# Kernel tuning notes

Hardware: AMD Instinct MI355X
Metric: run time of the kernel (lower is better)

Reference implementation:

```python
import jax, jax.numpy as jnp
import numpy as np
from jax import lax

WD, H, B, SQ, SS, CL = 300, 100, 128, 48, 48, 16
VOCAB, CVOCAB, CD, K = 91557, 53, 16, 3


def setup_inputs() -> dict:
    key = jax.random.key(0)
    ks = jax.random.split(key, 40)
    p = lambda i, shape: jax.random.normal(ks[i], shape, jnp.float32) * 0.02
    inp = {
        'q_words': jax.random.randint(ks[0], (B, SQ), 0, VOCAB),
        'q_chars': jax.random.randint(ks[1], (B, SQ, CL), 0, CVOCAB),
        's_words': jax.random.randint(ks[2], (B, SS), 0, VOCAB),
        's_chars': jax.random.randint(ks[3], (B, SS, CL), 0, CVOCAB),
        'word_emb': p(4, (VOCAB, WD)),
        'char_emb': p(5, (CVOCAB, CD)),
        'conv_w': p(6, (CD, 1, K)),
        'conv_b': p(7, (CD,)),
    }
    din = WD + CD
    for k in range(5):
        d = din + 2 * H * k  # dense connectivity: input grows by 2H per layer
        inp[f'wih{k+1}'] = p(8 + 4 * k, (4 * H, d))
        inp[f'whh{k+1}'] = p(9 + 4 * k, (4 * H, H))
        inp[f'bih{k+1}'] = p(10 + 4 * k, (4 * H,))
        inp[f'bhh{k+1}'] = p(11 + 4 * k, (4 * H,))
    inp['fcl_w'] = p(30, (800, 5 * H))
    inp['fcl_b'] = p(31, (800,))
    inp['last_w'] = p(32, (2, 800))
    inp['last_b'] = p(33, (2,))
    return inp


def _lstm_scan(x, wih, whh, bih, bhh):
    # x: [S, B, D] -> hidden states [S, B, H]; zero initial state (PyTorch LSTMCell default)
    h0 = jnp.zeros((x.shape[1], H), x.dtype)
    def step(carry, xt):
        h, c = carry
        g = xt @ wih.T + bih + h @ whh.T + bhh
        i, f, gg, o = jnp.split(g, 4, axis=-1)
        c = jax.nn.sigmoid(f) * c + jax.nn.sigmoid(i) * jnp.tanh(gg)
        h = jax.nn.sigmoid(o) * jnp.tanh(c)
        return (h, c), h
    _, hs = lax.scan(step, (h0, h0), x)
    return hs


def _embed(words, chars, word_emb, char_emb, conv_w, conv_b):
    w_e = word_emb[words]  # [B, S, WD]
    Bn, S, Cl = chars.shape
    ce = char_emb[chars].reshape(Bn * S, 1, Cl * CD)  # flatten chars per token
    raw = lax.conv_general_dilated(ce, conv_w, (1,), 'VALID',
                                   dimension_numbers=('NCH', 'OIH', 'NCH'))
    raw = (raw + conv_b[None, :, None]).reshape(Bn, S, CD, -1)
    pooled = jnp.max(jax.nn.relu(raw), axis=-1)        # [B, S, CD]
    pooled0 = jnp.max(raw[0], axis=-1)                 # original quirk: batch row 0 has no relu
    char_e = pooled.at[0].set(pooled0)
    return jnp.concatenate([w_e, char_e], axis=2).transpose(1, 0, 2)  # [S, B, WD+CD]


def _forward(q_words, q_chars, s_words, s_chars, word_emb, char_emb, conv_w, conv_b,
             cells, fcl_w, fcl_b, last_w, last_b):
    px = _embed(q_words, q_chars, word_emb, char_emb, conv_w, conv_b)
    hx = _embed(s_words, s_chars, word_emb, char_emb, conv_w, conv_b)
    hps = hhs = None
    for (wih, whh, bih, bhh) in cells:
        p_h = _lstm_scan(px, wih, whh, bih, bhh)  # [Sp, B, H]
        h_h = _lstm_scan(hx, wih, whh, bih, bhh)  # [Sh, B, H]
        hps = p_h.transpose(1, 0, 2)              # [B, Sp, H]
        hhs = h_h.transpose(1, 0, 2)              # [B, Sh, H]
        attn = jnp.einsum('bph,bqh->bpq', hps, hhs)
        a_p = jnp.einsum('bpq,bqh->bph', jax.nn.softmax(attn, axis=2), hhs)
        a_h = jnp.einsum('bqp,bph->bqh', jax.nn.softmax(attn.transpose(0, 2, 1), axis=2), hps)
        px = jnp.concatenate([px, a_p.transpose(1, 0, 2), p_h], axis=2)
        hx = jnp.concatenate([hx, a_h.transpose(1, 0, 2), h_h], axis=2)
    hq = jnp.max(hps, axis=1)  # max-pool over time
    hs = jnp.max(hhs, axis=1)
    feats = jnp.concatenate([hq, hs, hs - hq, hq * hs, jnp.abs(hq - hs)], axis=1)
    out = jax.nn.relu(feats @ fcl_w.T + fcl_b) @ last_w.T + last_b
    return jax.nn.sigmoid(out)


def reference(q_words, q_chars, s_words, s_chars, word_emb, char_emb, conv_w, conv_b,
              wih1, whh1, bih1, bhh1, wih2, whh2, bih2, bhh2, wih3, whh3, bih3, bhh3,
              wih4, whh4, bih4, bhh4, wih5, whh5, bih5, bhh5,
              fcl_w, fcl_b, last_w, last_b):
    cells = [(wih1, whh1, bih1, bhh1), (wih2, whh2, bih2, bhh2), (wih3, whh3, bih3, bhh3),
             (wih4, whh4, bih4, bhh4), (wih5, whh5, bih5, bhh5)]
    return _forward(q_words, q_chars, s_words, s_chars, word_emb, char_emb, conv_w, conv_b,
                    cells, fcl_w, fcl_b, last_w, last_b)
```

## Files before the change

kernel.cpp:

```cpp
#include <hip/hip_runtime.h>

typedef unsigned short u16;
typedef unsigned int   u32;

#define B_   128
#define S_   48
#define H_   100
#define G_   400
#define PXP  1120

__device__ __forceinline__ float b2f(u16 u) {
    union { u32 i; float f; } v; v.i = ((u32)u) << 16; return v.f;
}
__device__ __forceinline__ u16 f2b(float f) {
    union { float f; u32 i; } v; v.f = f;
    u32 r = v.i + 0x7FFF + ((v.i >> 16) & 1);
    return (u16)(r >> 16);
}
__device__ __forceinline__ float sigf(float x) { return 1.f / (1.f + expf(-x)); }

__device__ __forceinline__ float fsig(float x) { return 1.f / (1.f + __expf(-x)); }
__device__ __forceinline__ float ftanh(float x) {
    const float t = __expf(-2.f * fabsf(x));
    const float r = (1.f - t) / (1.f + t);
    return copysignf(r, x);
}

__device__ __forceinline__ float rl(float v0, float v1, int u) {
    return __int_as_float(
        u < 64 ? __builtin_amdgcn_readlane(__float_as_int(v0), u)
               : __builtin_amdgcn_readlane(__float_as_int(v1), u - 64));
}

__device__ __forceinline__ float ldw(const void* p, long i, int bf) {
    return bf ? b2f(((const u16*)p)[i]) : ((const float*)p)[i];
}

__global__ __launch_bounds__(256) void detect_kernel(const void* wemb, int* flag)
{
    const int t = threadIdx.x;
    __shared__ int s;
    if (t == 0) s = 0;
    __syncthreads();
    int bad = 0;
    const u16* p = (const u16*)wemb;
    for (int i = t; i < 4096; i += 256) {
        float v = b2f(p[i]);
        if (!(fabsf(v) < 1e4f)) bad = 1;
    }
    if (bad) atomicOr(&s, 1);
    __syncthreads();
    if (t == 0) *flag = s ? 0 : 1;
}

__global__ __launch_bounds__(64) void embed_kernel(
    const int* __restrict__ qw, const int* __restrict__ qc,
    const int* __restrict__ sw, const int* __restrict__ sc,
    const void* __restrict__ wemb, const void* __restrict__ cemb,
    const void* __restrict__ cw, const void* __restrict__ cb,
    u16* __restrict__ px, u16* __restrict__ hx, const int* __restrict__ flagp)
{
    const int bf = *flagp;
    const int b = blockIdx.x, s = blockIdx.y, seq = blockIdx.z;
    const int* words = seq ? sw : qw;
    const int* chars = seq ? sc : qc;
    u16* dst = seq ? hx : px;
    const int t = threadIdx.x;

    u16* row = dst + (long)(s * B_ + b) * PXP;
    const int w = words[b * S_ + s];
    if (bf) {
        const u16* src = (const u16*)wemb + (long)w * 300;
        for (int d = t; d < 300; d += 64) row[d] = src[d];
    } else {
        const float* src = (const float*)wemb + (long)w * 300;
        for (int d = t; d < 300; d += 64) row[d] = f2b(src[d]);
    }

    __shared__ float ce[256];
    const int* ch = chars + (b * S_ + s) * 16;
    for (int j = t; j < 256; j += 64) {
        int ci = ch[j >> 4];
        ce[j] = ldw(cemb, ci * 16 + (j & 15), bf);
    }
    __syncthreads();

    float cwr[3][16], cbr[16];
#pragma unroll
    for (int oc = 0; oc < 16; ++oc) {
        cbr[oc] = ldw(cb, oc, bf);
#pragma unroll
        for (int kk = 0; kk < 3; ++kk) cwr[kk][oc] = ldw(cw, oc * 3 + kk, bf);
    }

    float vmax[16];
#pragma unroll
    for (int oc = 0; oc < 16; ++oc) vmax[oc] = -1e30f;

    for (int p = t; p < 254; p += 64) {
        float c0 = ce[p], c1 = ce[p + 1], c2 = ce[p + 2];
#pragma unroll
        for (int oc = 0; oc < 16; ++oc) {
            float v = fmaf(c0, cwr[0][oc], fmaf(c1, cwr[1][oc], fmaf(c2, cwr[2][oc], cbr[oc])));
            vmax[oc] = fmaxf(vmax[oc], v);
        }
    }
#pragma unroll
    for (int m = 32; m; m >>= 1) {
#pragma unroll
        for (int oc = 0; oc < 16; ++oc)
            vmax[oc] = fmaxf(vmax[oc], __shfl_xor(vmax[oc], m));
    }
    if (t == 0) {
#pragma unroll
        for (int oc = 0; oc < 16; ++oc) {
            float v = vmax[oc];
            if (b != 0) v = fmaxf(v, 0.f);
            row[300 + oc] = f2b(v);
        }
    }
}

#if defined(__gfx950__)

typedef __attribute__((ext_vector_type(4))) float f32x4;
typedef __attribute__((ext_vector_type(8))) __bf16 bf16x8;
#define LDP 72

__global__ __launch_bounds__(256) void gemm_wih(
    const u16* __restrict__ px, const u16* __restrict__ hx,
    float* __restrict__ Xg_p, float* __restrict__ Xg_h,
    const void* __restrict__ wih, const void* __restrict__ bih,
    const void* __restrict__ bhh, int K, const int* __restrict__ flagp)
{
    const int bf = *flagp;
    const u16* A = blockIdx.z ? hx : px;
    float* C = blockIdx.z ? Xg_h : Xg_p;
    const int m0 = blockIdx.x * 128, n0 = blockIdx.y * 64;

    __shared__ __align__(16) u16 As[128 * LDP];
    __shared__ __align__(16) u16 Bs[64 * LDP];

    const int tid = threadIdx.x;
    const int ra = tid >> 1;
    const int ka = (tid & 1) * 32;
    const int rb = tid >> 2;
    const int kb = (tid & 3) * 16;

    const int lane = tid & 63;
    const int w    = tid >> 6;
    const int fr   = lane & 15;
    const int fq   = lane >> 4;

    const u16* wp = (const u16*)wih;

    f32x4 acc[2][4] = {};

    for (int k0 = 0; k0 < K; k0 += 64) {
        u16* as = &As[ra * LDP + ka];
        u16* bs = &Bs[rb * LDP + kb];
        const int n = n0 + rb;
        if (k0 + 64 <= K) {
            const u16* ap = A + (long)(m0 + ra) * PXP + k0 + ka;
#pragma unroll
            for (int c = 0; c < 4; ++c)
                *(float4*)(as + c * 8) = *(const float4*)(ap + c * 8);
            if (n < G_) {
                const u16* bp = wp + (long)n * K + k0 + kb;
#pragma unroll
                for (int c = 0; c < 4; ++c)
                    *(uint2*)(bs + c * 4) = *(const uint2*)(bp + c * 4);
            } else {
#pragma unroll
                for (int i = 0; i < 16; ++i) bs[i] = 0;
            }
        } else {
            const u16* ar = A + (long)(m0 + ra) * PXP;
            const u16* br = wp + (long)n * K;
            const int nok = n < G_;
#pragma unroll
            for (int i = 0; i < 32; ++i) {
                const int k = k0 + ka + i;
                as[i] = (k < K) ? ar[k] : (u16)0;
            }
#pragma unroll
            for (int i = 0; i < 16; ++i) {
                const int k = k0 + kb + i;
                bs[i] = (nok && k < K) ? br[k] : (u16)0;
            }
        }
        __syncthreads();

#pragma unroll
        for (int ks = 0; ks < 64; ks += 32) {
            bf16x8 a0 = *(const bf16x8*)&As[(w * 32 + fr) * LDP + ks + fq * 8];
            bf16x8 a1 = *(const bf16x8*)&As[(w * 32 + 16 + fr) * LDP + ks + fq * 8];
#pragma unroll
            for (int j = 0; j < 4; ++j) {
                bf16x8 bj = *(const bf16x8*)&Bs[(j * 16 + fr) * LDP + ks + fq * 8];
                acc[0][j] = __builtin_amdgcn_mfma_f32_16x16x32_bf16(a0, bj, acc[0][j], 0, 0, 0);
                acc[1][j] = __builtin_amdgcn_mfma_f32_16x16x32_bf16(a1, bj, acc[1][j], 0, 0, 0);
            }
        }
        __syncthreads();
    }

#pragma unroll
    for (int j = 0; j < 4; ++j) {
        const int col = n0 + j * 16 + fr;
        if (col < G_) {
            const float bias = ldw(bih, col, bf) + ldw(bhh, col, bf);
#pragma unroll
            for (int m = 0; m < 2; ++m)
#pragma unroll
                for (int i = 0; i < 4; ++i) {
                    const int row = m0 + w * 32 + m * 16 + fq * 4 + i;
                    C[(long)row * G_ + col] = acc[m][j][i] + bias;
                }
        }
    }
}
#undef LDP

#else

__global__ __launch_bounds__(256) void gemm_wih(
    const u16* __restrict__ px, const u16* __restrict__ hx,
    float* __restrict__ Xg_p, float* __restrict__ Xg_h,
    const void* __restrict__ wih, const void* __restrict__ bih,
    const void* __restrict__ bhh, int K, const int* __restrict__ flagp)
{
    const int bf = *flagp;
    const u16* A = blockIdx.z ? hx : px;
    float* C = blockIdx.z ? Xg_h : Xg_p;

    __shared__ float As[16][64];
    __shared__ float Bs[16][64];

    const int tid = threadIdx.x;
    const int tx = tid & 15, ty = tid >> 4;
    const int m0 = blockIdx.x * 64, n0 = blockIdx.y * 64;
    const int lr = tid >> 2, lk = (tid & 3) * 4;

    float acc[4][4] = {};

    for (int k0 = 0; k0 < K; k0 += 16) {
        const u16* Ap = A + (long)(m0 + lr) * PXP + k0 + lk;
#pragma unroll
        for (int u = 0; u < 4; ++u)
            As[lk + u][lr] = (k0 + lk + u < K) ? b2f(Ap[u]) : 0.f;
        {
            const int n = n0 + lr;
#pragma unroll
            for (int u = 0; u < 4; ++u) {
                const int kk = k0 + lk + u;
                Bs[lk + u][lr] = (n < G_ && kk < K) ? ldw(wih, (long)n * K + kk, bf) : 0.f;
            }
        }
        __syncthreads();
#pragma unroll
        for (int k = 0; k < 16; ++k) {
            float a[4], bq[4];
#pragma unroll
            for (int i = 0; i < 4; ++i) a[i] = As[k][ty * 4 + i];
#pragma unroll
            for (int j = 0; j < 4; ++j) bq[j] = Bs[k][tx * 4 + j];
#pragma unroll
            for (int i = 0; i < 4; ++i)
#pragma unroll
                for (int j = 0; j < 4; ++j)
                    acc[i][j] = fmaf(a[i], bq[j], acc[i][j]);
        }
        __syncthreads();
    }

#pragma unroll
    for (int j = 0; j < 4; ++j) {
        const int col = n0 + tx * 4 + j;
        if (col < G_) {
            const float bias = ldw(bih, col, bf) + ldw(bhh, col, bf);
#pragma unroll
            for (int i = 0; i < 4; ++i)
                C[(long)(m0 + ty * 4 + i) * G_ + col] = acc[i][j] + bias;
        }
    }
}

#endif

__global__ __launch_bounds__(448, 2)
void lstm_scan(
    const float* __restrict__ Xg_p, const float* __restrict__ Xg_h,
    const void* __restrict__ whh,
    float* __restrict__ p_h, float* __restrict__ h_h,
    u16* __restrict__ px, u16* __restrict__ hx, int cat_off,
    const int* __restrict__ flagp)
{
    const int bf = *flagp;
    const int b = blockIdx.x, seq = blockIdx.y;
    const float* Xg = seq ? Xg_h : Xg_p;
    float* hout = seq ? h_h : p_h;
    u16* xcat = seq ? hx : px;
    const int g = threadIdx.x;
    const int l = g & 63;

    __shared__ float h_lds[128];
    __shared__ float g_lds[400];
    __shared__ float h_hist[S_ * 104];

    u32 wpk[50];
    float xg = 0.f;
    if (g < G_) {
        if (bf) {
            const u32* w2 = (const u32*)whh;
#pragma unroll
            for (int j = 0; j < 50; ++j) wpk[j] = w2[g * 50 + j];
        } else {
            const float* wf = (const float*)whh;
#pragma unroll
            for (int j = 0; j < 50; ++j) {
                u32 lo = f2b(wf[(long)g * 100 + 2 * j]);
                u32 hi = f2b(wf[(long)g * 100 + 2 * j + 1]);
                wpk[j] = lo | (hi << 16);
            }
        }
#pragma unroll
        for (int j = 0; j < 50; ++j) asm volatile("" : "+v"(wpk[j]));
        xg = Xg[(long)b * G_ + g];
    }
    if (g < 128) h_lds[g] = 0.f;
    float c_reg = 0.f;
    __syncthreads();

    for (int s = 0; s < S_; ++s) {
        const float hv0 = h_lds[l];
        const float hv1 = h_lds[l + 64];
        if (g < G_) {
            float a0 = xg, a1 = 0.f, a2 = 0.f, a3 = 0.f;
#pragma unroll
            for (int u = 0; u < 100; u += 4) {
                const u32 p0 = wpk[u >> 1], p1 = wpk[(u >> 1) + 1];
                const float w0 = __int_as_float(p0 << 16);
                const float w1 = __int_as_float(p0 & 0xFFFF0000u);
                const float w2 = __int_as_float(p1 << 16);
                const float w3 = __int_as_float(p1 & 0xFFFF0000u);
                a0 = fmaf(rl(hv0, hv1, u),     w0, a0);
                a1 = fmaf(rl(hv0, hv1, u + 1), w1, a1);
                a2 = fmaf(rl(hv0, hv1, u + 2), w2, a2);
                a3 = fmaf(rl(hv0, hv1, u + 3), w3, a3);
            }
            g_lds[g] = (a0 + a1) + (a2 + a3);
            if (s + 1 < S_) xg = Xg[(long)((s + 1) * B_ + b) * G_ + g];
        }
        __syncthreads();
        if (g < H_) {
            const float iv = fsig(g_lds[g]);
            const float fv = fsig(g_lds[100 + g]);
            const float gv = ftanh(g_lds[200 + g]);
            const float ov = fsig(g_lds[300 + g]);
            c_reg = fv * c_reg + iv * gv;
            const float hv = ov * ftanh(c_reg);
            h_lds[g] = hv;
            h_hist[s * 104 + g] = hv;
        }
        __syncthreads();
    }

    for (int i = g; i < S_ * H_; i += 448) {
        const int s = i / H_, d = i - s * H_;
        const float hv = h_hist[s * 104 + d];
        hout[(long)(s * B_ + b) * H_ + d] = hv;
        if (cat_off >= 0) xcat[(long)(s * B_ + b) * PXP + cat_off + d] = f2b(hv);
    }
}

__global__ __launch_bounds__(256) void attn_kernel(
    const float* __restrict__ p_h, const float* __restrict__ h_h,
    u16* __restrict__ px, u16* __restrict__ hx, int off)
{
    const int b = blockIdx.x, t = threadIdx.x;
    __shared__ float P[4800], Q[4800], A[2304], Sx[2304];

    for (int i = t; i < 4800; i += 256) {
        const int s = i / 100, d = i % 100;
        P[i] = p_h[(long)(s * B_ + b) * H_ + d];
        Q[i] = h_h[(long)(s * B_ + b) * H_ + d];
    }
    __syncthreads();

    for (int e = t; e < 2304; e += 256) {
        const int p = e / 48, q = e % 48;
        float acc = 0.f;
        for (int j = 0; j < 100; ++j) acc = fmaf(P[p * 100 + j], Q[q * 100 + j], acc);
        A[e] = acc;
    }
    __syncthreads();

    if (t < 48) {
        float m = -1e30f;
        for (int q = 0; q < 48; ++q) m = fmaxf(m, A[t * 48 + q]);
        float sum = 0.f;
        for (int q = 0; q < 48; ++q) sum += expf(A[t * 48 + q] - m);
        const float inv = 1.f / sum;
        for (int q = 0; q < 48; ++q) Sx[t * 48 + q] = expf(A[t * 48 + q] - m) * inv;
    }
    __syncthreads();

    for (int e = t; e < 4800; e += 256) {
        const int p = e / 100, d = e % 100;
        float acc = 0.f;
        for (int q = 0; q < 48; ++q) acc = fmaf(Sx[p * 48 + q], Q[q * 100 + d], acc);
        px[(long)(p * B_ + b) * PXP + off + d] = f2b(acc);
    }
    __syncthreads();

    if (t < 48) {
        float m = -1e30f;
        for (int p = 0; p < 48; ++p) m = fmaxf(m, A[p * 48 + t]);
        float sum = 0.f;
        for (int p = 0; p < 48; ++p) sum += expf(A[p * 48 + t] - m);
        const float inv = 1.f / sum;
        for (int p = 0; p < 48; ++p) Sx[p * 48 + t] = expf(A[p * 48 + t] - m) * inv;
    }
    __syncthreads();

    for (int e = t; e < 4800; e += 256) {
        const int q = e / 100, d = e % 100;
        float acc = 0.f;
        for (int p = 0; p < 48; ++p) acc = fmaf(Sx[p * 48 + q], P[p * 100 + d], acc);
        hx[(long)(q * B_ + b) * PXP + off + d] = f2b(acc);
    }
}

__global__ __launch_bounds__(256) void pool_feats(
    const float* __restrict__ p_h, const float* __restrict__ h_h,
    float* __restrict__ feats)
{
    const int t = blockIdx.x * 256 + threadIdx.x;
    if (t >= B_ * H_) return;
    const int b = t / H_, u = t % H_;
    float hq = -1e30f, hs = -1e30f;
    for (int s = 0; s < S_; ++s) {
        hq = fmaxf(hq, p_h[(long)(s * B_ + b) * H_ + u]);
        hs = fmaxf(hs, h_h[(long)(s * B_ + b) * H_ + u]);
    }
    float* f = feats + b * 500;
    f[u]       = hq;
    f[100 + u] = hs;
    f[200 + u] = hs - hq;
    f[300 + u] = hq * hs;
    f[400 + u] = fabsf(hq - hs);
}

__global__ __launch_bounds__(256) void fcl_kernel(
    const float* __restrict__ feats, const void* __restrict__ fw,
    const void* __restrict__ fb, float* __restrict__ z, const int* __restrict__ flagp)
{
    const int bf = *flagp;
    const int t = blockIdx.x * 256 + threadIdx.x;
    const int o = t >> 7, b = t & 127;
    float acc = ldw(fb, o, bf);
    const float* f = feats + b * 500;
    for (int d = 0; d < 500; ++d) acc = fmaf(f[d], ldw(fw, (long)o * 500 + d, bf), acc);
    z[b * 800 + o] = fmaxf(acc, 0.f);
}

__global__ __launch_bounds__(256) void last_kernel(
    const float* __restrict__ z, const void* __restrict__ lw,
    const void* __restrict__ lb, void* __restrict__ out, const int* __restrict__ flagp)
{
    const int bf = *flagp;
    const int t = threadIdx.x;
    const int b = t >> 1, c = t & 1;
    float acc = ldw(lb, c, bf);
    const float* zr = z + b * 800;
    for (int o = 0; o < 800; ++o) acc = fmaf(zr[o], ldw(lw, (long)c * 800 + o, bf), acc);
    const float v = 1.f / (1.f + expf(-acc));
    if (bf) ((u16*)out)[t] = f2b(v);
    else    ((float*)out)[t] = v;
}

extern "C" void kernel_launch(void* const* d_in, const int* in_sizes, int n_in,
                              void* d_out, int out_size, void* d_ws, size_t ws_size,
                              hipStream_t stream)
{
    (void)in_sizes; (void)n_in; (void)out_size; (void)ws_size;

    const int* qw = (const int*)d_in[0];
    const int* qc = (const int*)d_in[1];
    const int* sw = (const int*)d_in[2];
    const int* sc = (const int*)d_in[3];
    const void* wemb = d_in[4];
    const void* cemb = d_in[5];
    const void* cw   = d_in[6];
    const void* cb   = d_in[7];
    const void* fclw = d_in[28];
    const void* fclb = d_in[29];
    const void* lw   = d_in[30];
    const void* lb   = d_in[31];

    float* ws = (float*)d_ws;
    int*  flag = (int*)ws;
    u16* px   = (u16*)(ws + 16);
    u16* hx   = px + (long)S_ * B_ * PXP;
    float* Xg_p = (float*)(hx + (long)S_ * B_ * PXP);
    float* Xg_h = Xg_p + (long)S_ * B_ * G_;
    float* p_h  = Xg_h + (long)S_ * B_ * G_;
    float* h_h  = p_h + (long)S_ * B_ * H_;
    float* feats = h_h + (long)S_ * B_ * H_;
    float* z    = feats + B_ * 500;

    detect_kernel<<<dim3(1), 256, 0, stream>>>(wemb, flag);

    embed_kernel<<<dim3(B_, S_, 2), 64, 0, stream>>>(qw, qc, sw, sc, wemb, cemb, cw, cb, px, hx, flag);

    for (int k = 0; k < 5; ++k) {
        const void* wih = d_in[8 + 4 * k];
        const void* whh = d_in[9 + 4 * k];
        const void* bih = d_in[10 + 4 * k];
        const void* bhh = d_in[11 + 4 * k];
        const int K = 316 + 200 * k;

        gemm_wih<<<dim3(48, 7, 2), 256, 0, stream>>>(px, hx, Xg_p, Xg_h, wih, bih, bhh, K, flag);

        const int cat = (k < 4) ? (K + 100) : -1;
        lstm_scan<<<dim3(B_, 2), 448, 0, stream>>>(Xg_p, Xg_h, whh, p_h, h_h, px, hx, cat, flag);

        if (k < 4)
            attn_kernel<<<dim3(B_), 256, 0, stream>>>(p_h, h_h, px, hx, K);
    }

    pool_feats<<<dim3(50), 256, 0, stream>>>(p_h, h_h, feats);
    fcl_kernel<<<dim3(400), 256, 0, stream>>>(feats, fclw, fclb, z, flag);
    last_kernel<<<dim3(1), 256, 0, stream>>>(z, lw, lb, d_out, flag);
}
```

Measured before the change: 976.6 us.

## Prefetch GEMM tiles via registers, widen embed copy, split attention by direction

```diff
diff --git a/kernel.cpp b/kernel.cpp
--- a/kernel.cpp
+++ b/kernel.cpp
@@ -70,8 +70,9 @@
     u16* row = dst + (long)(s * B_ + b) * PXP;
     const int w = words[b * S_ + s];
     if (bf) {
-        const u16* src = (const u16*)wemb + (long)w * 300;
-        for (int d = t; d < 300; d += 64) row[d] = src[d];
+        const u32* src = (const u32*)((const u16*)wemb + (long)w * 300);
+        u32* d32 = (u32*)row;
+        for (int d = t; d < 150; d += 64) d32[d] = src[d];
     } else {
         const float* src = (const float*)wemb + (long)w * 300;
         for (int d = t; d < 300; d += 64) row[d] = f2b(src[d]);
@@ -125,9 +126,10 @@
 
 typedef __attribute__((ext_vector_type(4))) float f32x4;
 typedef __attribute__((ext_vector_type(8))) __bf16 bf16x8;
-#define LDP 72
-
-__global__ __launch_bounds__(256) void gemm_wih(
+#define LDP 136
+#define BK  128
+
+__global__ __launch_bounds__(256, 3) void gemm_wih(
     const u16* __restrict__ px, const u16* __restrict__ hx,
     float* __restrict__ Xg_p, float* __restrict__ Xg_h,
     const void* __restrict__ wih, const void* __restrict__ bih,
@@ -143,9 +145,11 @@
 
     const int tid = threadIdx.x;
     const int ra = tid >> 1;
-    const int ka = (tid & 1) * 32;
+    const int ka = (tid & 1) * 64;
     const int rb = tid >> 2;
-    const int kb = (tid & 3) * 16;
+    const int kb = (tid & 3) * 32;
+    const int nB = n0 + rb;
+    const int bok = nB < G_;
 
     const int lane = tid & 63;
     const int w    = tid >> 6;
@@ -153,46 +157,50 @@
     const int fq   = lane >> 4;
 
     const u16* wp = (const u16*)wih;
+    const u16* aSrc = A + (long)(m0 + ra) * PXP + ka;
+    const u16* bSrc = wp + (long)nB * K + kb;
 
     f32x4 acc[2][4] = {};
-
-    for (int k0 = 0; k0 < K; k0 += 64) {
-        u16* as = &As[ra * LDP + ka];
-        u16* bs = &Bs[rb * LDP + kb];
-        const int n = n0 + rb;
-        if (k0 + 64 <= K) {
-            const u16* ap = A + (long)(m0 + ra) * PXP + k0 + ka;
-#pragma unroll
-            for (int c = 0; c < 4; ++c)
-                *(float4*)(as + c * 8) = *(const float4*)(ap + c * 8);
-            if (n < G_) {
-                const u16* bp = wp + (long)n * K + k0 + kb;
-#pragma unroll
-                for (int c = 0; c < 4; ++c)
-                    *(uint2*)(bs + c * 4) = *(const uint2*)(bp + c * 4);
-            } else {
-#pragma unroll
-                for (int i = 0; i < 16; ++i) bs[i] = 0;
-            }
+    float4 aR[8];
+    uint2  bR[8];
+
+    const int nfull = K / BK;
+
+    if (nfull > 0) {
+#pragma unroll
+        for (int i = 0; i < 8; ++i) aR[i] = *(const float4*)(aSrc + i * 8);
+        if (bok) {
+#pragma unroll
+            for (int i = 0; i < 8; ++i) bR[i] = *(const uint2*)(bSrc + i * 4);
         } else {
-            const u16* ar = A + (long)(m0 + ra) * PXP;
-            const u16* br = wp + (long)n * K;
-            const int nok = n < G_;
-#pragma unroll
-            for (int i = 0; i < 32; ++i) {
-                const int k = k0 + ka + i;
-                as[i] = (k < K) ? ar[k] : (u16)0;
-            }
-#pragma unroll
-            for (int i = 0; i < 16; ++i) {
-                const int k = k0 + kb + i;
-                bs[i] = (nok && k < K) ? br[k] : (u16)0;
-            }
-        }
-        __syncthreads();
-
-#pragma unroll
-        for (int ks = 0; ks < 64; ks += 32) {
+#pragma unroll
+            for (int i = 0; i < 8; ++i) { bR[i].x = 0u; bR[i].y = 0u; }
+        }
+    }
+
+    for (int t = 0; t < nfull; ++t) {
+        __syncthreads();
+        {
+            u16* as = &As[ra * LDP + ka];
+            u16* bs = &Bs[rb * LDP + kb];
+#pragma unroll
+            for (int i = 0; i < 8; ++i) *(float4*)(as + i * 8) = aR[i];
+#pragma unroll
+            for (int i = 0; i < 8; ++i) *(uint2*)(bs + i * 4) = bR[i];
+        }
+        __syncthreads();
+        if (t + 1 < nfull) {
+            const u16* ap = aSrc + (t + 1) * BK;
+#pragma unroll
+            for (int i = 0; i < 8; ++i) aR[i] = *(const float4*)(ap + i * 8);
+            if (bok) {
+                const u16* bp = bSrc + (t + 1) * BK;
+#pragma unroll
+                for (int i = 0; i < 8; ++i) bR[i] = *(const uint2*)(bp + i * 4);
+            }
+        }
+#pragma unroll
+        for (int ks = 0; ks < BK; ks += 32) {
             bf16x8 a0 = *(const bf16x8*)&As[(w * 32 + fr) * LDP + ks + fq * 8];
             bf16x8 a1 = *(const bf16x8*)&As[(w * 32 + 16 + fr) * LDP + ks + fq * 8];
 #pragma unroll
@@ -202,7 +210,39 @@
                 acc[1][j] = __builtin_amdgcn_mfma_f32_16x16x32_bf16(a1, bj, acc[1][j], 0, 0, 0);
             }
         }
-        __syncthreads();
+    }
+
+    const int k0 = nfull * BK;
+    if (k0 < K) {
+        __syncthreads();
+        {
+            u16* as = &As[ra * LDP + ka];
+            u16* bs = &Bs[rb * LDP + kb];
+            const u16* ar = A + (long)(m0 + ra) * PXP;
+            const u16* br = wp + (long)nB * K;
+#pragma unroll
+            for (int i = 0; i < 64; ++i) {
+                const int k = k0 + ka + i;
+                as[i] = (k < K) ? ar[k] : (u16)0;
+            }
+#pragma unroll
+            for (int i = 0; i < 32; ++i) {
+                const int k = k0 + kb + i;
+                bs[i] = (bok && k < K) ? br[k] : (u16)0;
+            }
+        }
+        __syncthreads();
+#pragma unroll
+        for (int ks = 0; ks < BK; ks += 32) {
+            bf16x8 a0 = *(const bf16x8*)&As[(w * 32 + fr) * LDP + ks + fq * 8];
+            bf16x8 a1 = *(const bf16x8*)&As[(w * 32 + 16 + fr) * LDP + ks + fq * 8];
+#pragma unroll
+            for (int j = 0; j < 4; ++j) {
+                bf16x8 bj = *(const bf16x8*)&Bs[(j * 16 + fr) * LDP + ks + fq * 8];
+                acc[0][j] = __builtin_amdgcn_mfma_f32_16x16x32_bf16(a0, bj, acc[0][j], 0, 0, 0);
+                acc[1][j] = __builtin_amdgcn_mfma_f32_16x16x32_bf16(a1, bj, acc[1][j], 0, 0, 0);
+            }
+        }
     }
 
 #pragma unroll
@@ -221,6 +261,7 @@
     }
 }
 #undef LDP
+#undef BK
 
 #else
 
@@ -378,57 +419,69 @@
     const float* __restrict__ p_h, const float* __restrict__ h_h,
     u16* __restrict__ px, u16* __restrict__ hx, int off)
 {
-    const int b = blockIdx.x, t = threadIdx.x;
-    __shared__ float P[4800], Q[4800], A[2304], Sx[2304];
-
-    for (int i = t; i < 4800; i += 256) {
-        const int s = i / 100, d = i % 100;
-        P[i] = p_h[(long)(s * B_ + b) * H_ + d];
-        Q[i] = h_h[(long)(s * B_ + b) * H_ + d];
+    const int b = blockIdx.x, dir = blockIdx.y, t = threadIdx.x;
+    __shared__ __align__(16) float P[4800], Q[4800];
+    __shared__ float A[2304], Sx[2304];
+
+    {
+        float4* P4 = (float4*)P;
+        float4* Q4 = (float4*)Q;
+        for (int i = t; i < 1200; i += 256) {
+            const int s = i / 25, d4 = i % 25;
+            P4[i] = *(const float4*)(p_h + (long)(s * B_ + b) * H_ + d4 * 4);
+            Q4[i] = *(const float4*)(h_h + (long)(s * B_ + b) * H_ + d4 * 4);
+        }
     }
     __syncthreads();
 
     for (int e = t; e < 2304; e += 256) {
         const int p = e / 48, q = e % 48;
-        float acc = 0.f;
-        for (int j = 0; j < 100; ++j) acc = fmaf(P[p * 100 + j], Q[q * 100 + j], acc);
-        A[e] = acc;
+        const float4* Pr = (const float4*)&P[p * 100];
+        const float4* Qr = (const float4*)&Q[q * 100];
+        float a0 = 0.f, a1 = 0.f;
+#pragma unroll
+        for (int j = 0; j < 25; ++j) {
+            const float4 u = Pr[j], v = Qr[j];
+            a0 = fmaf(u.x, v.x, a0); a1 = fmaf(u.y, v.y, a1);
+            a0 = fmaf(u.z, v.z, a0); a1 = fmaf(u.w, v.w, a1);
+        }
+        A[e] = a0 + a1;
     }
     __syncthreads();
 
     if (t < 48) {
-        float m = -1e30f;
-        for (int q = 0; q < 48; ++q) m = fmaxf(m, A[t * 48 + q]);
-        float sum = 0.f;
-        for (int q = 0; q < 48; ++q) sum += expf(A[t * 48 + q] - m);
-        const float inv = 1.f / sum;
-        for (int q = 0; q < 48; ++q) Sx[t * 48 + q] = expf(A[t * 48 + q] - m) * inv;
-    }
-    __syncthreads();
-
-    for (int e = t; e < 4800; e += 256) {
-        const int p = e / 100, d = e % 100;
-        float acc = 0.f;
-        for (int q = 0; q < 48; ++q) acc = fmaf(Sx[p * 48 + q], Q[q * 100 + d], acc);
-        px[(long)(p * B_ + b) * PXP + off + d] = f2b(acc);
-    }
-    __syncthreads();
-
-    if (t < 48) {
-        float m = -1e30f;
-        for (int p = 0; p < 48; ++p) m = fmaxf(m, A[p * 48 + t]);
-        float sum = 0.f;
-        for (int p = 0; p < 48; ++p) sum += expf(A[p * 48 + t] - m);
-        const float inv = 1.f / sum;
-        for (int p = 0; p < 48; ++p) Sx[p * 48 + t] = expf(A[p * 48 + t] - m) * inv;
-    }
-    __syncthreads();
-
-    for (int e = t; e < 4800; e += 256) {
-        const int q = e / 100, d = e % 100;
-        float acc = 0.f;
-        for (int p = 0; p < 48; ++p) acc = fmaf(Sx[p * 48 + q], P[p * 100 + d], acc);
-        hx[(long)(q * B_ + b) * PXP + off + d] = f2b(acc);
+        if (dir == 0) {
+            float m = -1e30f;
+            for (int q = 0; q < 48; ++q) m = fmaxf(m, A[t * 48 + q]);
+            float sum = 0.f;
+            for (int q = 0; q < 48; ++q) sum += __expf(A[t * 48 + q] - m);
+            const float inv = 1.f / sum;
+            for (int q = 0; q < 48; ++q) Sx[t * 48 + q] = __expf(A[t * 48 + q] - m) * inv;
+        } else {
+            float m = -1e30f;
+            for (int p = 0; p < 48; ++p) m = fmaxf(m, A[p * 48 + t]);
+            float sum = 0.f;
+            for (int p = 0; p < 48; ++p) sum += __expf(A[p * 48 + t] - m);
+            const float inv = 1.f / sum;
+            for (int p = 0; p < 48; ++p) Sx[p * 48 + t] = __expf(A[p * 48 + t] - m) * inv;
+        }
+    }
+    __syncthreads();
+
+    if (dir == 0) {
+        for (int e = t; e < 4800; e += 256) {
+            const int p = e / 100, d = e % 100;
+            float acc = 0.f;
+            for (int q = 0; q < 48; ++q) acc = fmaf(Sx[p * 48 + q], Q[q * 100 + d], acc);
+            px[(long)(p * B_ + b) * PXP + off + d] = f2b(acc);
+        }
+    } else {
+        for (int e = t; e < 4800; e += 256) {
+            const int q = e / 100, d = e % 100;
+            float acc = 0.f;
+            for (int p = 0; p < 48; ++p) acc = fmaf(Sx[p * 48 + q], P[p * 100 + d], acc);
+            hx[(long)(q * B_ + b) * PXP + off + d] = f2b(acc);
+        }
     }
 }
 
@@ -527,7 +580,7 @@
         lstm_scan<<<dim3(B_, 2), 448, 0, stream>>>(Xg_p, Xg_h, whh, p_h, h_h, px, hx, cat, flag);
 
         if (k < 4)
-            attn_kernel<<<dim3(B_), 256, 0, stream>>>(p_h, h_h, px, hx, K);
+            attn_kernel<<<dim3(B_, 2), 256, 0, stream>>>(p_h, h_h, px, hx, K);
     }
 
     pool_feats<<<dim3(50), 256, 0, stream>>>(p_h, h_h, feats);
```

New measurement: 1.089 ms. +11.5%, slower.
